# Kernel optimization log

Hardware: AMD Instinct MI355X
Metric: run time of the kernel (lower is better)

## Reference

```python
import jax, jax.numpy as jnp
import numpy as np


def setup_inputs() -> dict:
    key = jax.random.key(0)
    k1, k2 = jax.random.split(key)
    b, feat = 8192, 256
    x = jax.random.normal(k1, (b, feat), dtype=jnp.float32)
    y = jax.random.randint(k2, (b,), 0, 100, dtype=jnp.int64)
    T = jnp.zeros((1,), dtype=jnp.float32)
    return {"x": x, "y": y, "T": T}


def reference(x, y, T):
    # SNNLoss.forward with inv=False, d=None, and no -1 labels in y
    b = x.shape[0]
    x = x / jnp.std(x, ddof=1)  # torch .std() is unbiased (ddof=1)

    # Pairwise Euclidean distance via Gram matrix (avoids [b,b,feat] blowup)
    sq = jnp.sum(x * x, axis=1)  # [b]
    d2 = jnp.maximum(sq[:, None] + sq[None, :] - 2.0 * (x @ x.T), 0.0)  # [b,b]
    eye = jnp.eye(b, dtype=bool)
    # diagonal is exactly 0 and masked out later; keep sqrt grad-safe there
    dist = jnp.where(eye, 0.0, jnp.sqrt(jnp.where(eye, 1.0, d2)))

    e_dist = -dist * jnp.power(jnp.float32(10.0), T[0])  # [b,b]
    neg_inf = jnp.float32(-jnp.inf)

    # denominator: all pairs except self
    den_dist = jnp.where(eye, neg_inf, e_dist)
    den = jax.scipy.special.logsumexp(den_dist, axis=1)  # [b]

    # numerator: same-label pairs except self
    m_num = (y[:, None] == y[None, :]) & ~eye  # [b,b]
    has = jnp.any(m_num, axis=1)  # rows with at least one positive
    num_dist = jnp.where(m_num, e_dist, neg_inf)
    # rows with no positives would give logsumexp = -inf; torch code zeroes
    # both num and den there. Substitute finite values, then zero the term.
    num = jax.scipy.special.logsumexp(jnp.where(has[:, None], num_dist, 0.0), axis=1)
    terms = jnp.where(has, num - den, 0.0)
    return -jnp.mean(terms)
```

## Files before the change

### kernel.cpp

```cpp
#include <hip/hip_runtime.h>

#define B_ROWS 8192
#define FEAT   256
#define NCCH   16
#define NJTILE 128

typedef float f32x4 __attribute__((ext_vector_type(4)));
typedef _Float16 f16x8 __attribute__((ext_vector_type(8)));

typedef const __attribute__((address_space(1))) unsigned int* gas_ptr;
typedef __attribute__((address_space(3))) unsigned int* las_ptr;

__device__ __forceinline__ void gload_lds16(const void* g, void* l) {
  __builtin_amdgcn_global_load_lds((gas_ptr)g, (las_ptr)l, 16, 0, 0);
}

__global__ __launch_bounds__(256) void prep_kernel(
    const float* __restrict__ x, unsigned short* __restrict__ xh,
    float* __restrict__ sq, float* __restrict__ part_s,
    float* __restrict__ part_q, float* __restrict__ col_den,
    float* __restrict__ col_num)
{
  int tid = threadIdx.x;
  int l = tid & 63, wid = tid >> 6;
  int row = blockIdx.x * 4 + wid;
  const float4* xv = (const float4*)(x + (size_t)row * FEAT);
  float4 v = xv[l];
  ushort4 u;
  u.x = __builtin_bit_cast(unsigned short, (_Float16)v.x);
  u.y = __builtin_bit_cast(unsigned short, (_Float16)v.y);
  u.z = __builtin_bit_cast(unsigned short, (_Float16)v.z);
  u.w = __builtin_bit_cast(unsigned short, (_Float16)v.w);
  ((ushort4*)(xh + (size_t)row * FEAT))[l] = u;
  if (tid < 4) {
    int r4 = blockIdx.x * 4 + tid;
    col_den[r4] = 0.f;
    col_num[r4] = 0.f;
  }
  float ssq  = v.x*v.x + v.y*v.y + v.z*v.z + v.w*v.w;
  float ssum = v.x + v.y + v.z + v.w;
  #pragma unroll
  for (int m = 32; m; m >>= 1) {
    ssq  += __shfl_xor(ssq, m);
    ssum += __shfl_xor(ssum, m);
  }
  if (l == 0) sq[row] = ssq;
  __shared__ float red[8];
  if (l == 0) { red[wid*2] = ssum; red[wid*2+1] = ssq; }
  __syncthreads();
  if (tid == 0) {
    part_s[blockIdx.x] = red[0]+red[2]+red[4]+red[6];
    part_q[blockIdx.x] = red[1]+red[3]+red[5]+red[7];
  }
}

template<bool DIAG, bool COL>
__device__ __forceinline__ void epilogue(
    const f32x4 (&acc)[2][4], const float* __restrict__ sq,
    const int* __restrict__ y, int j0, int l15, int l,
    int i0q, const float (&sqi)[8], const int (&yiv)[8],
    float (&sden)[8], float (&snum)[8], float nscale2,
    float* __restrict__ col_den, float* __restrict__ col_num)
{
  int jb = j0 + l15;
  float sqj[4]; int yj[4];
  #pragma unroll
  for (int cb = 0; cb < 4; ++cb) {
    int j = jb + cb*16;
    sqj[cb] = sq[j];
    yj[cb]  = y[j];
  }
  float cd[4], cn[4];
  if (COL) {
    #pragma unroll
    for (int cb = 0; cb < 4; ++cb) { cd[cb] = 0.f; cn[cb] = 0.f; }
  }
  #pragma unroll
  for (int rb = 0; rb < 2; ++rb) {
    #pragma unroll
    for (int r = 0; r < 4; ++r) {
      float si = sqi[rb*4+r];
      int   ig = i0q + rb*16 + r;
      int   yi = yiv[rb*4+r];
      float dacc = 0.f, nacc = 0.f;
      #pragma unroll
      for (int cb = 0; cb < 4; ++cb) {
        float S  = acc[rb][cb][r];
        float d2 = fmaf(S, -2.0f, si + sqj[cb]);
        d2 = fmaxf(d2, 0.0f);
        float e  = __builtin_amdgcn_exp2f(__builtin_amdgcn_sqrtf(d2) * nscale2);
        bool same = (yi == yj[cb]);
        bool offd = !DIAG || (ig != jb + cb*16);
        dacc += offd ? e : 0.0f;
        nacc += (same && offd) ? e : 0.0f;
        if (COL) {
          cd[cb] += e;
          cn[cb] += same ? e : 0.0f;
        }
      }
      sden[rb*4+r] += dacc;
      snum[rb*4+r] += nacc;
    }
  }
  if (COL) {
    #pragma unroll
    for (int cb = 0; cb < 4; ++cb) {
      cd[cb] += __shfl_xor(cd[cb], 16);
      cd[cb] += __shfl_xor(cd[cb], 32);
      cn[cb] += __shfl_xor(cn[cb], 16);
      cn[cb] += __shfl_xor(cn[cb], 32);
    }
    if (l < 16) {
      #pragma unroll
      for (int cb = 0; cb < 4; ++cb) {
        atomicAdd(&col_den[j0 + cb*16 + l], cd[cb]);
        atomicAdd(&col_num[j0 + cb*16 + l], cn[cb]);
      }
    }
  }
}

__device__ __forceinline__ void process_row(
    int it, int c, const char* __restrict__ xbc,
    const float* __restrict__ sq, const int* __restrict__ y,
    float nscale2, int l, int wid, int quad, int l15, int l5, int s31,
    float* __restrict__ pden, float* __restrict__ pnum,
    float* __restrict__ col_den, float* __restrict__ col_num,
    char* lB)
{
  int i0 = it * 128;

  f16x8 areg[2][8];
  #pragma unroll
  for (int rb = 0; rb < 2; ++rb)
    #pragma unroll
    for (int kk = 0; kk < 8; ++kk)
      areg[rb][kk] = *(const f16x8*)(xbc +
          (size_t)(i0 + wid*32 + rb*16 + l15)*512 + kk*64 + quad*16);

  float sqi[8]; int yiv[8];
  int i0q = i0 + wid*32 + quad*4;
  #pragma unroll
  for (int rb = 0; rb < 2; ++rb)
    #pragma unroll
    for (int r = 0; r < 4; ++r) {
      int idx = i0q + rb*16 + r;
      sqi[rb*4+r] = sq[idx];
      yiv[rb*4+r] = y[idx];
    }

  float sden[8], snum[8];
  #pragma unroll
  for (int v = 0; v < 8; ++v) { sden[v] = 0.f; snum[v] = 0.f; }
  f32x4 acc[2][4];
  const f32x4 zero4 = {0.f, 0.f, 0.f, 0.f};

  int f = 2*it + ((c - 2*it) & (NCCH-1));
  int pjt = -1;

  for (int jt = f; jt < NJTILE; jt += NCCH) {
    int j0 = jt * 64;

    __syncthreads();
    {
      const char* gB = xbc + (size_t)j0 * 512;
      #pragma unroll
      for (int s = 0; s < 8; ++s) {
        int cc = wid*8 + s;
        int rw = 2*cc + l5;
        int gg = s31 ^ (rw & 7);
        gload_lds16(gB + rw*512 + gg*16, lB + cc*1024);
      }
    }

    if (pjt >= 0) {
      int pj0 = pjt * 64;
      if ((pjt >> 1) == it)
        epilogue<true , false>(acc, sq, y, pj0, l15, l, i0q, sqi, yiv,
                               sden, snum, nscale2, col_den, col_num);
      else
        epilogue<false, true >(acc, sq, y, pj0, l15, l, i0q, sqi, yiv,
                               sden, snum, nscale2, col_den, col_num);
    }
    #pragma unroll
    for (int rb = 0; rb < 2; ++rb)
      #pragma unroll
      for (int cb = 0; cb < 4; ++cb)
        acc[rb][cb] = zero4;

    __syncthreads();

    #pragma unroll
    for (int kk = 0; kk < 8; ++kk) {
      f16x8 bv[4];
      #pragma unroll
      for (int cb = 0; cb < 4; ++cb) {
        int nr = cb*16 + l15;
        bv[cb] = *(const f16x8*)(lB + nr*512 + ((((kk<<2)|quad) ^ (l15 & 7)) << 4));
      }
      #pragma unroll
      for (int rb = 0; rb < 2; ++rb)
        #pragma unroll
        for (int cb = 0; cb < 4; ++cb)
          acc[rb][cb] = __builtin_amdgcn_mfma_f32_16x16x32_f16(areg[rb][kk], bv[cb], acc[rb][cb], 0, 0, 0);
    }
    pjt = jt;
  }
  if (pjt >= 0) {
    int pj0 = pjt * 64;
    if ((pjt >> 1) == it)
      epilogue<true , false>(acc, sq, y, pj0, l15, l, i0q, sqi, yiv,
                             sden, snum, nscale2, col_den, col_num);
    else
      epilogue<false, true >(acc, sq, y, pj0, l15, l, i0q, sqi, yiv,
                             sden, snum, nscale2, col_den, col_num);
  }

  #pragma unroll
  for (int v = 0; v < 8; ++v) {
    #pragma unroll
    for (int m = 1; m <= 8; m <<= 1) {
      sden[v] += __shfl_xor(sden[v], m);
      snum[v] += __shfl_xor(snum[v], m);
    }
  }
  if (l15 == 0) {
    int base = (it*NCCH + c) * 128;
    #pragma unroll
    for (int rb = 0; rb < 2; ++rb)
      #pragma unroll
      for (int r = 0; r < 4; ++r) {
        int rin = wid*32 + rb*16 + quad*4 + r;
        pden[base + rin] = sden[rb*4+r];
        pnum[base + rin] = snum[rb*4+r];
      }
  }
}

__global__ __launch_bounds__(256, 2) void snn_main(
    const unsigned short* __restrict__ xh, const float* __restrict__ sq,
    const int* __restrict__ y, const float* __restrict__ T,
    const float* __restrict__ part_s, const float* __restrict__ part_q,
    float* __restrict__ pden, float* __restrict__ pnum,
    float* __restrict__ col_den, float* __restrict__ col_num)
{
  __shared__ __align__(16) char lB[32768];
  int tid = threadIdx.x;
  int l = tid & 63, wid = tid >> 6;
  int quad = l >> 4, l15 = l & 15;
  int l5 = l >> 5, s31 = l & 31;
  int c = blockIdx.x, p = blockIdx.y;
  const char* xbc = (const char*)xh;

  float s_acc = 0.f, q_acc = 0.f;
  #pragma unroll
  for (int t = 0; t < 32; ++t) {
    s_acc += part_s[l + 64*t];
    q_acc += part_q[l + 64*t];
  }
  #pragma unroll
  for (int m = 1; m <= 32; m <<= 1) {
    s_acc += __shfl_xor(s_acc, m);
    q_acc += __shfl_xor(q_acc, m);
  }
  const double n = (double)B_ROWS * FEAT;
  double var = ((double)q_acc - (double)s_acc*(double)s_acc/n) / (n - 1.0);
  float stdv = (float)sqrt(var);
  float p10  = __builtin_amdgcn_exp2f(T[0] * 3.3219280948873623f);
  float nscale2 = -(p10 * 1.4426950408889634f / stdv);

  process_row(p,      c, xbc, sq, y, nscale2, l, wid, quad, l15, l5, s31,
              pden, pnum, col_den, col_num, lB);
  process_row(63 - p, c, xbc, sq, y, nscale2, l, wid, quad, l15, l5, s31,
              pden, pnum, col_den, col_num, lB);
}

__global__ __launch_bounds__(1024) void final_kernel(
    const float* __restrict__ pden, const float* __restrict__ pnum,
    const float* __restrict__ col_den, const float* __restrict__ col_num,
    float* __restrict__ out)
{
  int tid = threadIdx.x;
  float tot = 0.f;
  #pragma unroll
  for (int rr = 0; rr < 8; ++rr) {
    int row = tid + 1024*rr;
    int itt = row >> 7, rin = row & 127;
    float den = col_den[row], num = col_num[row];
    #pragma unroll
    for (int p = 0; p < NCCH; ++p) {
      den += pden[(itt*NCCH + p)*128 + rin];
      num += pnum[(itt*NCCH + p)*128 + rin];
    }
    if (num > 0.f)
      tot += 0.6931471805599453f *
             (__builtin_amdgcn_logf(num) - __builtin_amdgcn_logf(den));
  }
  #pragma unroll
  for (int m = 32; m; m >>= 1) tot += __shfl_xor(tot, m);
  __shared__ float red[16];
  if ((tid & 63) == 0) red[tid >> 6] = tot;
  __syncthreads();
  if (tid == 0) {
    float s = 0.f;
    #pragma unroll
    for (int w = 0; w < 16; ++w) s += red[w];
    out[0] = -s / 8192.0f;
  }
}

extern "C" void kernel_launch(void* const* d_in, const int* in_sizes, int n_in,
                              void* d_out, int out_size, void* d_ws, size_t ws_size,
                              hipStream_t stream)
{
  (void)in_sizes; (void)n_in; (void)out_size; (void)ws_size;
  const float* x  = (const float*)d_in[0];
  const int* y    = (const int*)d_in[1];
  const float* T  = (const float*)d_in[2];
  char* ws = (char*)d_ws;
  float* part_s = (float*)(ws + 1024);
  float* part_q = (float*)(ws + 1024 + 8192);
  float* sq     = (float*)(ws + 32768);
  unsigned short* xh = (unsigned short*)(ws + 65536);
  float* pden   = (float*)(ws + 65536 + 4194304);
  float* pnum   = pden + 64*NCCH*128;
  float* col_den = pnum + 64*NCCH*128;
  float* col_num = col_den + B_ROWS;

  hipLaunchKernelGGL(prep_kernel, dim3(B_ROWS/4), dim3(256), 0, stream,
                     x, xh, sq, part_s, part_q, col_den, col_num);
  hipLaunchKernelGGL(snn_main, dim3(NCCH, 32), dim3(256), 0, stream,
                     xh, sq, y, T, part_s, part_q, pden, pnum, col_den, col_num);
  hipLaunchKernelGGL(final_kernel, dim3(1), dim3(1024), 0, stream,
                     pden, pnum, col_den, col_num, (float*)d_out);
}
```

Measured before the change: 121.9 us.

## Fuse paired row-tile passes to share each loaded B tile across both row blocks

The two sequential passes over row tiles p and 63-p are merged into one loop, so each B column tile loaded into LDS feeds MFMAs for both row blocks. This halves the LDS tile loads and barriers per block. Row sums now go through per-tile shuffles and atomics into row_den/row_num instead of per-thread register accumulators and a partial-sum buffer, which also simplifies the final reduction. In exchange it holds two sets of A fragments and accumulators in registers (pressure under launch_bounds 256,2) and issues many more global atomics.

```diff
diff --git a/kernel.cpp b/kernel.cpp
--- a/kernel.cpp
+++ b/kernel.cpp
@@ -19,7 +19,8 @@
     const float* __restrict__ x, unsigned short* __restrict__ xh,
     float* __restrict__ sq, float* __restrict__ part_s,
     float* __restrict__ part_q, float* __restrict__ col_den,
-    float* __restrict__ col_num)
+    float* __restrict__ col_num, float* __restrict__ row_den,
+    float* __restrict__ row_num)
 {
   int tid = threadIdx.x;
   int l = tid & 63, wid = tid >> 6;
@@ -34,8 +35,8 @@
   ((ushort4*)(xh + (size_t)row * FEAT))[l] = u;
   if (tid < 4) {
     int r4 = blockIdx.x * 4 + tid;
-    col_den[r4] = 0.f;
-    col_num[r4] = 0.f;
+    col_den[r4] = 0.f; col_num[r4] = 0.f;
+    row_den[r4] = 0.f; row_num[r4] = 0.f;
   }
   float ssq  = v.x*v.x + v.y*v.y + v.z*v.z + v.w*v.w;
   float ssum = v.x + v.y + v.z + v.w;
@@ -58,8 +59,8 @@
 __device__ __forceinline__ void epilogue(
     const f32x4 (&acc)[2][4], const float* __restrict__ sq,
     const int* __restrict__ y, int j0, int l15, int l,
-    int i0q, const float (&sqi)[8], const int (&yiv)[8],
-    float (&sden)[8], float (&snum)[8], float nscale2,
+    int rbase, float nscale2,
+    float* __restrict__ row_den, float* __restrict__ row_num,
     float* __restrict__ col_den, float* __restrict__ col_num)
 {
   int jb = j0 + l15;
@@ -79,9 +80,9 @@
   for (int rb = 0; rb < 2; ++rb) {
     #pragma unroll
     for (int r = 0; r < 4; ++r) {
-      float si = sqi[rb*4+r];
-      int   ig = i0q + rb*16 + r;
-      int   yi = yiv[rb*4+r];
+      int   ig = rbase + rb*16 + r;
+      float si = sq[ig];
+      int   yi = y[ig];
       float dacc = 0.f, nacc = 0.f;
       #pragma unroll
       for (int cb = 0; cb < 4; ++cb) {
@@ -98,8 +99,15 @@
           cn[cb] += same ? e : 0.0f;
         }
       }
-      sden[rb*4+r] += dacc;
-      snum[rb*4+r] += nacc;
+      #pragma unroll
+      for (int m = 1; m <= 8; m <<= 1) {
+        dacc += __shfl_xor(dacc, m);
+        nacc += __shfl_xor(nacc, m);
+      }
+      if (l15 == 0) {
+        atomicAdd(&row_den[ig], dacc);
+        atomicAdd(&row_num[ig], nacc);
+      }
     }
   }
   if (COL) {
@@ -120,128 +128,11 @@
   }
 }
 
-__device__ __forceinline__ void process_row(
-    int it, int c, const char* __restrict__ xbc,
-    const float* __restrict__ sq, const int* __restrict__ y,
-    float nscale2, int l, int wid, int quad, int l15, int l5, int s31,
-    float* __restrict__ pden, float* __restrict__ pnum,
-    float* __restrict__ col_den, float* __restrict__ col_num,
-    char* lB)
-{
-  int i0 = it * 128;
-
-  f16x8 areg[2][8];
-  #pragma unroll
-  for (int rb = 0; rb < 2; ++rb)
-    #pragma unroll
-    for (int kk = 0; kk < 8; ++kk)
-      areg[rb][kk] = *(const f16x8*)(xbc +
-          (size_t)(i0 + wid*32 + rb*16 + l15)*512 + kk*64 + quad*16);
-
-  float sqi[8]; int yiv[8];
-  int i0q = i0 + wid*32 + quad*4;
-  #pragma unroll
-  for (int rb = 0; rb < 2; ++rb)
-    #pragma unroll
-    for (int r = 0; r < 4; ++r) {
-      int idx = i0q + rb*16 + r;
-      sqi[rb*4+r] = sq[idx];
-      yiv[rb*4+r] = y[idx];
-    }
-
-  float sden[8], snum[8];
-  #pragma unroll
-  for (int v = 0; v < 8; ++v) { sden[v] = 0.f; snum[v] = 0.f; }
-  f32x4 acc[2][4];
-  const f32x4 zero4 = {0.f, 0.f, 0.f, 0.f};
-
-  int f = 2*it + ((c - 2*it) & (NCCH-1));
-  int pjt = -1;
-
-  for (int jt = f; jt < NJTILE; jt += NCCH) {
-    int j0 = jt * 64;
-
-    __syncthreads();
-    {
-      const char* gB = xbc + (size_t)j0 * 512;
-      #pragma unroll
-      for (int s = 0; s < 8; ++s) {
-        int cc = wid*8 + s;
-        int rw = 2*cc + l5;
-        int gg = s31 ^ (rw & 7);
-        gload_lds16(gB + rw*512 + gg*16, lB + cc*1024);
-      }
-    }
-
-    if (pjt >= 0) {
-      int pj0 = pjt * 64;
-      if ((pjt >> 1) == it)
-        epilogue<true , false>(acc, sq, y, pj0, l15, l, i0q, sqi, yiv,
-                               sden, snum, nscale2, col_den, col_num);
-      else
-        epilogue<false, true >(acc, sq, y, pj0, l15, l, i0q, sqi, yiv,
-                               sden, snum, nscale2, col_den, col_num);
-    }
-    #pragma unroll
-    for (int rb = 0; rb < 2; ++rb)
-      #pragma unroll
-      for (int cb = 0; cb < 4; ++cb)
-        acc[rb][cb] = zero4;
-
-    __syncthreads();
-
-    #pragma unroll
-    for (int kk = 0; kk < 8; ++kk) {
-      f16x8 bv[4];
-      #pragma unroll
-      for (int cb = 0; cb < 4; ++cb) {
-        int nr = cb*16 + l15;
-        bv[cb] = *(const f16x8*)(lB + nr*512 + ((((kk<<2)|quad) ^ (l15 & 7)) << 4));
-      }
-      #pragma unroll
-      for (int rb = 0; rb < 2; ++rb)
-        #pragma unroll
-        for (int cb = 0; cb < 4; ++cb)
-          acc[rb][cb] = __builtin_amdgcn_mfma_f32_16x16x32_f16(areg[rb][kk], bv[cb], acc[rb][cb], 0, 0, 0);
-    }
-    pjt = jt;
-  }
-  if (pjt >= 0) {
-    int pj0 = pjt * 64;
-    if ((pjt >> 1) == it)
-      epilogue<true , false>(acc, sq, y, pj0, l15, l, i0q, sqi, yiv,
-                             sden, snum, nscale2, col_den, col_num);
-    else
-      epilogue<false, true >(acc, sq, y, pj0, l15, l, i0q, sqi, yiv,
-                             sden, snum, nscale2, col_den, col_num);
-  }
-
-  #pragma unroll
-  for (int v = 0; v < 8; ++v) {
-    #pragma unroll
-    for (int m = 1; m <= 8; m <<= 1) {
-      sden[v] += __shfl_xor(sden[v], m);
-      snum[v] += __shfl_xor(snum[v], m);
-    }
-  }
-  if (l15 == 0) {
-    int base = (it*NCCH + c) * 128;
-    #pragma unroll
-    for (int rb = 0; rb < 2; ++rb)
-      #pragma unroll
-      for (int r = 0; r < 4; ++r) {
-        int rin = wid*32 + rb*16 + quad*4 + r;
-        pden[base + rin] = sden[rb*4+r];
-        pnum[base + rin] = snum[rb*4+r];
-      }
-  }
-}
-
 __global__ __launch_bounds__(256, 2) void snn_main(
     const unsigned short* __restrict__ xh, const float* __restrict__ sq,
     const int* __restrict__ y, const float* __restrict__ T,
     const float* __restrict__ part_s, const float* __restrict__ part_q,
-    float* __restrict__ pden, float* __restrict__ pnum,
+    float* __restrict__ row_den, float* __restrict__ row_num,
     float* __restrict__ col_den, float* __restrict__ col_num)
 {
   __shared__ __align__(16) char lB[32768];
@@ -250,7 +141,20 @@
   int quad = l >> 4, l15 = l & 15;
   int l5 = l >> 5, s31 = l & 31;
   int c = blockIdx.x, p = blockIdx.y;
+  int q = 63 - p;
+  int i0p = p * 128, i0q = q * 128;
+  int jq0 = 2 * q;
   const char* xbc = (const char*)xh;
+
+  f16x8 aregp[2][8], aregq[2][8];
+  #pragma unroll
+  for (int rb = 0; rb < 2; ++rb)
+    #pragma unroll
+    for (int kk = 0; kk < 8; ++kk) {
+      size_t off = (size_t)(wid*32 + rb*16 + l15)*512 + kk*64 + quad*16;
+      aregp[rb][kk] = *(const f16x8*)(xbc + (size_t)i0p*512 + off);
+      aregq[rb][kk] = *(const f16x8*)(xbc + (size_t)i0q*512 + off);
+    }
 
   float s_acc = 0.f, q_acc = 0.f;
   #pragma unroll
@@ -269,14 +173,102 @@
   float p10  = __builtin_amdgcn_exp2f(T[0] * 3.3219280948873623f);
   float nscale2 = -(p10 * 1.4426950408889634f / stdv);
 
-  process_row(p,      c, xbc, sq, y, nscale2, l, wid, quad, l15, l5, s31,
-              pden, pnum, col_den, col_num, lB);
-  process_row(63 - p, c, xbc, sq, y, nscale2, l, wid, quad, l15, l5, s31,
-              pden, pnum, col_den, col_num, lB);
+  int rbasep = i0p + wid*32 + quad*4;
+  int rbaseq = i0q + wid*32 + quad*4;
+
+  f32x4 accp[2][4], accq[2][4];
+  const f32x4 zero4 = {0.f, 0.f, 0.f, 0.f};
+
+  int f = 2*p + ((c - 2*p) & (NCCH-1));
+  int pjt = -1; bool ppq = false;
+
+  for (int jt = f; jt < NJTILE; jt += NCCH) {
+    int j0 = jt * 64;
+
+    __syncthreads();
+    {
+      const char* gB = xbc + (size_t)j0 * 512;
+      #pragma unroll
+      for (int s = 0; s < 8; ++s) {
+        int cc = wid*8 + s;
+        int rw = 2*cc + l5;
+        int gg = s31 ^ (rw & 7);
+        gload_lds16(gB + rw*512 + gg*16, lB + cc*1024);
+      }
+    }
+
+    if (pjt >= 0) {
+      int pj0 = pjt * 64;
+      if ((pjt >> 1) == p)
+        epilogue<true , false>(accp, sq, y, pj0, l15, l, rbasep, nscale2,
+                               row_den, row_num, col_den, col_num);
+      else
+        epilogue<false, true >(accp, sq, y, pj0, l15, l, rbasep, nscale2,
+                               row_den, row_num, col_den, col_num);
+      if (ppq) {
+        if ((pjt >> 1) == q)
+          epilogue<true , false>(accq, sq, y, pj0, l15, l, rbaseq, nscale2,
+                                 row_den, row_num, col_den, col_num);
+        else
+          epilogue<false, true >(accq, sq, y, pj0, l15, l, rbaseq, nscale2,
+                                 row_den, row_num, col_den, col_num);
+      }
+    }
+    #pragma unroll
+    for (int rb = 0; rb < 2; ++rb)
+      #pragma unroll
+      for (int cb = 0; cb < 4; ++cb) {
+        accp[rb][cb] = zero4;
+        accq[rb][cb] = zero4;
+      }
+
+    __syncthreads();
+
+    bool qact = (jt >= jq0);
+    #pragma unroll
+    for (int kk = 0; kk < 8; ++kk) {
+      f16x8 bv[4];
+      #pragma unroll
+      for (int cb = 0; cb < 4; ++cb) {
+        int nr = cb*16 + l15;
+        bv[cb] = *(const f16x8*)(lB + nr*512 + ((((kk<<2)|quad) ^ (l15 & 7)) << 4));
+      }
+      #pragma unroll
+      for (int rb = 0; rb < 2; ++rb)
+        #pragma unroll
+        for (int cb = 0; cb < 4; ++cb)
+          accp[rb][cb] = __builtin_amdgcn_mfma_f32_16x16x32_f16(aregp[rb][kk], bv[cb], accp[rb][cb], 0, 0, 0);
+      if (qact) {
+        #pragma unroll
+        for (int rb = 0; rb < 2; ++rb)
+          #pragma unroll
+          for (int cb = 0; cb < 4; ++cb)
+            accq[rb][cb] = __builtin_amdgcn_mfma_f32_16x16x32_f16(aregq[rb][kk], bv[cb], accq[rb][cb], 0, 0, 0);
+      }
+    }
+    pjt = jt; ppq = qact;
+  }
+  {
+    int pj0 = pjt * 64;
+    if ((pjt >> 1) == p)
+      epilogue<true , false>(accp, sq, y, pj0, l15, l, rbasep, nscale2,
+                             row_den, row_num, col_den, col_num);
+    else
+      epilogue<false, true >(accp, sq, y, pj0, l15, l, rbasep, nscale2,
+                             row_den, row_num, col_den, col_num);
+    if (ppq) {
+      if ((pjt >> 1) == q)
+        epilogue<true , false>(accq, sq, y, pj0, l15, l, rbaseq, nscale2,
+                               row_den, row_num, col_den, col_num);
+      else
+        epilogue<false, true >(accq, sq, y, pj0, l15, l, rbaseq, nscale2,
+                               row_den, row_num, col_den, col_num);
+    }
+  }
 }
 
 __global__ __launch_bounds__(1024) void final_kernel(
-    const float* __restrict__ pden, const float* __restrict__ pnum,
+    const float* __restrict__ row_den, const float* __restrict__ row_num,
     const float* __restrict__ col_den, const float* __restrict__ col_num,
     float* __restrict__ out)
 {
@@ -285,13 +277,8 @@
   #pragma unroll
   for (int rr = 0; rr < 8; ++rr) {
     int row = tid + 1024*rr;
-    int itt = row >> 7, rin = row & 127;
-    float den = col_den[row], num = col_num[row];
-    #pragma unroll
-    for (int p = 0; p < NCCH; ++p) {
-      den += pden[(itt*NCCH + p)*128 + rin];
-      num += pnum[(itt*NCCH + p)*128 + rin];
-    }
+    float den = row_den[row] + col_den[row];
+    float num = row_num[row] + col_num[row];
     if (num > 0.f)
       tot += 0.6931471805599453f *
              (__builtin_amdgcn_logf(num) - __builtin_amdgcn_logf(den));
@@ -322,15 +309,17 @@
   float* part_q = (float*)(ws + 1024 + 8192);
   float* sq     = (float*)(ws + 32768);
   unsigned short* xh = (unsigned short*)(ws + 65536);
-  float* pden   = (float*)(ws + 65536 + 4194304);
-  float* pnum   = pden + 64*NCCH*128;
-  float* col_den = pnum + 64*NCCH*128;
+  float* col_den = (float*)(ws + 65536 + 4194304);
   float* col_num = col_den + B_ROWS;
+  float* row_den = col_num + B_ROWS;
+  float* row_num = row_den + B_ROWS;
 
   hipLaunchKernelGGL(prep_kernel, dim3(B_ROWS/4), dim3(256), 0, stream,
-                     x, xh, sq, part_s, part_q, col_den, col_num);
+                     x, xh, sq, part_s, part_q, col_den, col_num,
+                     row_den, row_num);
   hipLaunchKernelGGL(snn_main, dim3(NCCH, 32), dim3(256), 0, stream,
-                     xh, sq, y, T, part_s, part_q, pden, pnum, col_den, col_num);
+                     xh, sq, y, T, part_s, part_q, row_den, row_num,
+                     col_den, col_num);
   hipLaunchKernelGGL(final_kernel, dim3(1), dim3(1024), 0, stream,
-                     pden, pnum, col_den, col_num, (float*)d_out);
-}
+                     row_den, row_num, col_den, col_num, (float*)d_out);
+}
```

New measurement: 184.0 us. 1.51x slower.
